# Performance work log

Measured on AMD Instinct MI355X. Metric: run time of the kernel, lower is better.

## Reference

```python
import jax, jax.numpy as jnp
import numpy as np

B, IN_F, OUT_F, H = 2048, 512, 512, 8
D = OUT_F // H  # head_dim = 64


def setup_inputs() -> dict:
    key = jax.random.key(0)
    ks = jax.random.split(key, 4)
    x = jax.random.normal(ks[0], (B, IN_F), dtype=jnp.float32)
    # learned params (per init_kwargs): nn.Linear(IN_F, OUT_F) and attention vector a
    W_w = jax.random.normal(ks[1], (OUT_F, IN_F), dtype=jnp.float32) * (1.0 / np.sqrt(IN_F))
    W_b = jnp.zeros((OUT_F,), dtype=jnp.float32)
    a = jax.random.normal(ks[2], (2 * D, 1), dtype=jnp.float32) * 0.1
    adj = jax.random.randint(ks[3], (B, B), 0, 2, dtype=jnp.int32)
    return {"x": x, "adj": adj, "W_w": W_w, "W_b": W_b, "a": a}


def reference(x, adj, W_w, W_b, a):
    Bn = x.shape[0]
    # h: [B, H, D]
    h = (x @ W_w.T + W_b).reshape(Bn, H, D)
    # decompose shared attention vector into src/dst halves (same for every head,
    # since torch code tiles a across heads via a.repeat(1, num_heads))
    a_src, a_dst = a[:D, 0], a[D:, 0]
    s_src = jnp.einsum('bhd,d->bh', h, a_src)  # [B, H] contribution of node i
    s_dst = jnp.einsum('bhd,d->bh', h, a_dst)  # [B, H] contribution of node j
    # e[i, j, h] = leakyrelu(h_i . a_src + h_j . a_dst)  -> [B, B, H]
    e = jax.nn.leaky_relu(s_src[:, None, :] + s_dst[None, :, :], negative_slope=0.2)
    e = jnp.where(adj[:, :, None] == 0, jnp.float32(-1e9), e)
    attn = jax.nn.softmax(e, axis=1)  # softmax over neighbors j (torch dim=1)
    # h_prime[i, h, :] = sum_j attn[i, j, h] * h[j, h, :]
    h_prime = jnp.einsum('ijh,jhd->ihd', attn, h).reshape(Bn, H * D)
    return jax.nn.elu(h_prime)
```

## Files before the change

### kernel.cpp

```cpp
#include <hip/hip_runtime.h>
#include <hip/hip_bf16.h>
#include <math.h>
#include <stdint.h>

#define BN 2048
#define KF 512
#define OF 512
#define NH 8
#define DD 64

typedef __attribute__((ext_vector_type(8))) short short8;
typedef __attribute__((ext_vector_type(4))) float f32x4;
typedef unsigned short ushortT;

static __device__ __forceinline__ ushortT bfcvt(float f) {
  __hip_bfloat16 h = __float2bfloat16(f);
  return *reinterpret_cast<ushortT*>(&h);
}
static __device__ __forceinline__ float bf2f(ushortT b) {
  return __uint_as_float(((unsigned)b) << 16);
}

#define SPLIT8(vsrc, dhi, dlo)                                        \
  {                                                                   \
    ushortT hi8[8], lo8[8];                                           \
    _Pragma("unroll") for (int i = 0; i < 8; ++i) {                   \
      hi8[i] = bfcvt((vsrc)[i]);                                      \
      lo8[i] = bfcvt((vsrc)[i] - bf2f(hi8[i]));                       \
    }                                                                 \
    (dhi) = *(const int4*)hi8;                                        \
    (dlo) = *(const int4*)lo8;                                        \
  }

__global__ __launch_bounds__(256, 2) void k_main(
    const float* __restrict__ x, const int* __restrict__ adj,
    const float* __restrict__ W, const float* __restrict__ Wb,
    const float* __restrict__ av,
    ushortT* __restrict__ hF, float* __restrict__ E12s, float* __restrict__ E12d,
    uint8_t* __restrict__ adjB) {
  __shared__ __align__(16) uint8_t smem[24576];
  __shared__ float sredS[2][32], sredD[2][32];

  const int t    = threadIdx.x;
  const int hh   = blockIdx.x;
  const int i0   = blockIdx.y * 32;
  const int b    = hh * 64 + blockIdx.y;
  const int lane = t & 63;
  const int wv   = t >> 6;
  const int mt   = wv & 1;
  const int nt   = wv >> 1;
  const int l15  = lane & 15;
  const int lq   = lane >> 4;

  {
    const int gtid = b * 256 + t;
#pragma unroll
    for (int it = 0; it < 4; ++it) {
      const int bidx = gtid + it * (512 * 256);
      const int4 v0 = *(const int4*)(adj + (size_t)bidx * 8);
      const int4 v1 = *(const int4*)(adj + (size_t)bidx * 8 + 4);
      unsigned m = (v0.x ? 1u : 0u) | (v0.y ? 2u : 0u) | (v0.z ? 4u : 0u) | (v0.w ? 8u : 0u)
                 | (v1.x ? 16u : 0u) | (v1.y ? 32u : 0u) | (v1.z ? 64u : 0u) | (v1.w ? 128u : 0u);
      adjB[bidx] = (uint8_t)m;
    }
  }

  ushortT* sAh = (ushortT*)smem;
  ushortT* sAl = sAh + 32 * 64;
  ushortT* sBh = sAl + 32 * 64;
  ushortT* sBl = sBh + 64 * 64;

  f32x4 acc[2] = {};
  const int srow = t >> 3, ss = t & 7;
  int4 aHi, aLo, bHi[2], bLo[2];

  {
    const float* xs = x + (size_t)(i0 + srow) * KF + ss * 8;
    float v[8];
    *(float4*)&v[0] = *(const float4*)xs;
    *(float4*)&v[4] = *(const float4*)(xs + 4);
    SPLIT8(v, aHi, aLo)
#pragma unroll
    for (int rp = 0; rp < 2; ++rp) {
      const int S = t + rp * 256, rw = S >> 3, s2 = S & 7;
      const float* wsrc = W + (size_t)(hh * 64 + rw) * KF + s2 * 8;
      float wv8[8];
      *(float4*)&wv8[0] = *(const float4*)wsrc;
      *(float4*)&wv8[4] = *(const float4*)(wsrc + 4);
      SPLIT8(wv8, bHi[rp], bLo[rp])
    }
  }

  for (int k0 = 0; k0 < 8; ++k0) {
    __syncthreads();
    {
      const int offA = srow * 64 + ((ss ^ (srow & 7)) * 8);
      *(int4*)&sAh[offA] = aHi;
      *(int4*)&sAl[offA] = aLo;
#pragma unroll
      for (int rp = 0; rp < 2; ++rp) {
        const int S = t + rp * 256, rw = S >> 3, s2 = S & 7;
        const int offB = rw * 64 + ((s2 ^ (rw & 7)) * 8);
        *(int4*)&sBh[offB] = bHi[rp];
        *(int4*)&sBl[offB] = bLo[rp];
      }
    }
    __syncthreads();
    if (k0 < 7) {
      const int kc = (k0 + 1) * 64;
      const float* xs = x + (size_t)(i0 + srow) * KF + kc + ss * 8;
      float v[8];
      *(float4*)&v[0] = *(const float4*)xs;
      *(float4*)&v[4] = *(const float4*)(xs + 4);
      SPLIT8(v, aHi, aLo)
#pragma unroll
      for (int rp = 0; rp < 2; ++rp) {
        const int S = t + rp * 256, rw = S >> 3, s2 = S & 7;
        const float* wsrc = W + (size_t)(hh * 64 + rw) * KF + kc + s2 * 8;
        float wv8[8];
        *(float4*)&wv8[0] = *(const float4*)wsrc;
        *(float4*)&wv8[4] = *(const float4*)(wsrc + 4);
        SPLIT8(wv8, bHi[rp], bLo[rp])
      }
    }
#pragma unroll
    for (int kb = 0; kb < 2; ++kb) {
      const int sc = kb * 4 + lq;
      const int arow = mt * 16 + l15;
      const int offA = arow * 64 + ((sc ^ (arow & 7)) * 8);
      const short8 afh = *(const short8*)&sAh[offA];
      const short8 afl = *(const short8*)&sAl[offA];
      const int br0 = nt * 32 + l15;
      const int br1 = br0 + 16;
      const int offB0 = br0 * 64 + ((sc ^ (br0 & 7)) * 8);
      const int offB1 = br1 * 64 + ((sc ^ (br1 & 7)) * 8);
      const short8 bh0 = *(const short8*)&sBh[offB0];
      const short8 bl0 = *(const short8*)&sBl[offB0];
      const short8 bh1 = *(const short8*)&sBh[offB1];
      const short8 bl1 = *(const short8*)&sBl[offB1];
      acc[0] = __builtin_amdgcn_mfma_f32_16x16x32_bf16(afh, bh0, acc[0], 0, 0, 0);
      acc[1] = __builtin_amdgcn_mfma_f32_16x16x32_bf16(afh, bh1, acc[1], 0, 0, 0);
      acc[0] = __builtin_amdgcn_mfma_f32_16x16x32_bf16(afh, bl0, acc[0], 0, 0, 0);
      acc[1] = __builtin_amdgcn_mfma_f32_16x16x32_bf16(afh, bl1, acc[1], 0, 0, 0);
      acc[0] = __builtin_amdgcn_mfma_f32_16x16x32_bf16(afl, bh0, acc[0], 0, 0, 0);
      acc[1] = __builtin_amdgcn_mfma_f32_16x16x32_bf16(afl, bh1, acc[1], 0, 0, 0);
    }
  }

  __syncthreads();
  ushortT* ldsT = (ushortT*)smem;
  float bias2[2], asv[2], adv[2];
#pragma unroll
  for (int bb = 0; bb < 2; ++bb) {
    const int fl = nt * 32 + bb * 16 + l15;
    bias2[bb] = Wb[hh * 64 + fl];
    asv[bb] = av[fl];
    adv[bb] = av[DD + fl];
  }
#pragma unroll
  for (int p = 0; p < 4; ++p) {
    float vs = 0.f, vd = 0.f;
#pragma unroll
    for (int bb = 0; bb < 2; ++bb) {
      const float hv = acc[bb][p] + bias2[bb];
      const ushortT hu = bfcvt(hv);
      vs = fmaf(hv, asv[bb], vs);
      vd = fmaf(hv, adv[bb], vd);
      ldsT[(nt * 32 + bb * 16 + l15) * 40 + mt * 16 + lq * 4 + p] = hu;
    }
    vs += __shfl_xor(vs, 1); vs += __shfl_xor(vs, 2);
    vs += __shfl_xor(vs, 4); vs += __shfl_xor(vs, 8);
    vd += __shfl_xor(vd, 1); vd += __shfl_xor(vd, 2);
    vd += __shfl_xor(vd, 4); vd += __shfl_xor(vd, 8);
    if (l15 == 0) {
      sredS[nt][mt * 16 + lq * 4 + p] = vs;
      sredD[nt][mt * 16 + lq * 4 + p] = vd;
    }
  }
  __syncthreads();
  if (t < 32) {
    const float s1 = sredS[0][t] + sredS[1][t];
    const float s2 = sredD[0][t] + sredD[1][t];
    const size_t gi = (size_t)hh * BN + i0 + t;
    float2 sv; sv.x = __expf(s1); sv.y = __expf(0.2f * s1);
    float2 dv; dv.x = __expf(s2); dv.y = __expf(0.2f * s2);
    *(float2*)&E12s[gi * 2] = sv;
    *(float2*)&E12d[gi * 2] = dv;
  }
  {
    const int n = t >> 6, ln = t & 63;
    const int4 v = *(const int4*)&ldsT[(n * 16 + (ln & 15)) * 40 + ((ln >> 4) * 8)];
    const size_t chunk = (((size_t)hh * 64 + blockIdx.y) * 4 + n) * 64 + ln;
    *(int4*)&hF[chunk * 8] = v;
  }
}

__global__ __launch_bounds__(512, 4) void k_attn(
    const ushortT* __restrict__ hF, const uint8_t* __restrict__ adjB,
    const float* __restrict__ E12s, const float* __restrict__ E12d,
    float* __restrict__ out) {
  __shared__ __align__(16) float e12[BN * 2];
  __shared__ __align__(16) float cbuf[4][2 * 16 * 68];
  __shared__ uint8_t abits[32 * 272];
  __shared__ float denP[8][2][16];

  const int t    = threadIdx.x;
  const int hh   = blockIdx.x;
  const int i0   = blockIdx.y * 32;
  const int lane = t & 63;
  const int wv   = t >> 6;
  const int l15  = lane & 15;
  const int lq   = lane >> 4;

  {
    const float4* g = (const float4*)(E12d + (size_t)hh * BN * 2);
    ((float4*)e12)[t]       = g[t];
    ((float4*)e12)[t + 512] = g[t + 512];
    const int r = t >> 4, pp = t & 15;
    *(int4*)(abits + r * 272 + pp * 16) =
        *(const int4*)(adjB + (size_t)(i0 + r) * 256 + pp * 16);
  }

  const float2 eiA = *(const float2*)&E12s[2 * ((size_t)hh * BN + i0 + l15)];
  const float2 eiB = *(const float2*)&E12s[2 * ((size_t)hh * BN + i0 + 16 + l15)];

  const short8 ones8 = {(short)0x3F80, (short)0x3F80, (short)0x3F80, (short)0x3F80,
                        (short)0x3F80, (short)0x3F80, (short)0x3F80, (short)0x3F80};

  const ushortT* hfb = hF + (size_t)hh * 131072 + (size_t)lane * 8;

  __syncthreads();

  const uint4 wA0 = *(const uint4*)(abits + l15 * 272 + wv * 32);
  const uint4 wA1 = *(const uint4*)(abits + l15 * 272 + wv * 32 + 16);
  const uint4 wB0 = *(const uint4*)(abits + (16 + l15) * 272 + wv * 32);
  const uint4 wB1 = *(const uint4*)(abits + (16 + l15) * 272 + wv * 32 + 16);
  const int lqs = lq * 8;

  f32x4 acc0[4] = {}, acc1[4] = {};
  f32x4 accd0 = {0.f, 0.f, 0.f, 0.f}, accd1 = {0.f, 0.f, 0.f, 0.f};

  const int jb0 = wv * 8;
  short8 bfA[4], bfB[4];
  {
    const ushortT* b0 = hfb + (size_t)(jb0 * 4) * 512;
#pragma unroll
    for (int n = 0; n < 4; ++n) bfA[n] = *(const short8*)(b0 + (size_t)n * 512);
  }

#define WSEL0(s) ((s)==0?wA0.x:(s)==1?wA0.y:(s)==2?wA0.z:(s)==3?wA0.w: \
                  (s)==4?wA1.x:(s)==5?wA1.y:(s)==6?wA1.z:wA1.w)
#define WSEL1(s) ((s)==0?wB0.x:(s)==1?wB0.y:(s)==2?wB0.z:(s)==3?wB0.w: \
                  (s)==4?wB1.x:(s)==5?wB1.y:(s)==6?wB1.z:wB1.w)

#define STEP(s, BCUR, BNXT)                                                        \
  {                                                                                \
    if ((s) < 7) {                                                                 \
      const ushortT* bn = hfb + (size_t)((jb0 + (s) + 1) * 4) * 512;               \
      _Pragma("unroll") for (int n = 0; n < 4; ++n)                                \
        BNXT[n] = *(const short8*)(bn + (size_t)n * 512);                          \
    }                                                                              \
    const int j0 = (jb0 + (s)) * 32 + lq * 8;                                      \
    const float* ep = &e12[j0 * 2];                                                \
    const float4 r0 = *(const float4*)(ep);                                        \
    const float4 r1 = *(const float4*)(ep + 4);                                    \
    const float4 r2 = *(const float4*)(ep + 8);                                    \
    const float4 r3 = *(const float4*)(ep + 12);                                   \
    const unsigned bb0 = (WSEL0(s) >> lqs) & 0xffu;                                \
    const unsigned bb1 = (WSEL1(s) >> lqs) & 0xffu;                                \
    unsigned pk0[4], pk1[4];                                                       \
    _Pragma("unroll") for (int q = 0; q < 4; ++q) {                                \
      const float4 rq = (q == 0) ? r0 : (q == 1) ? r1 : (q == 2) ? r2 : r3;        \
      float wa0 = fmaxf(eiA.x * rq.x, eiA.y * rq.y);                               \
      float wb0 = fmaxf(eiA.x * rq.z, eiA.y * rq.w);                               \
      float wa1 = fmaxf(eiB.x * rq.x, eiB.y * rq.y);                               \
      float wb1 = fmaxf(eiB.x * rq.z, eiB.y * rq.w);                               \
      wa0 = ((bb0 >> (2 * q)) & 1u) ? wa0 : 0.f;                                   \
      wb0 = ((bb0 >> (2 * q + 1)) & 1u) ? wb0 : 0.f;                               \
      wa1 = ((bb1 >> (2 * q)) & 1u) ? wa1 : 0.f;                                   \
      wb1 = ((bb1 >> (2 * q + 1)) & 1u) ? wb1 : 0.f;                               \
      asm("v_cvt_pk_bf16_f32 %0, %1, %2" : "=v"(pk0[q]) : "v"(wa0), "v"(wb0));     \
      asm("v_cvt_pk_bf16_f32 %0, %1, %2" : "=v"(pk1[q]) : "v"(wa1), "v"(wb1));     \
    }                                                                              \
    const short8 af0 = *(const short8*)pk0;                                        \
    const short8 af1 = *(const short8*)pk1;                                        \
    _Pragma("unroll") for (int n = 0; n < 4; ++n) {                                \
      acc0[n] = __builtin_amdgcn_mfma_f32_16x16x32_bf16(af0, BCUR[n], acc0[n], 0, 0, 0); \
      acc1[n] = __builtin_amdgcn_mfma_f32_16x16x32_bf16(af1, BCUR[n], acc1[n], 0, 0, 0); \
    }                                                                              \
    accd0 = __builtin_amdgcn_mfma_f32_16x16x32_bf16(af0, ones8, accd0, 0, 0, 0);   \
    accd1 = __builtin_amdgcn_mfma_f32_16x16x32_bf16(af1, ones8, accd1, 0, 0, 0);   \
  }

  STEP(0, bfA, bfB) STEP(1, bfB, bfA) STEP(2, bfA, bfB) STEP(3, bfB, bfA)
  STEP(4, bfA, bfB) STEP(5, bfB, bfA) STEP(6, bfA, bfB) STEP(7, bfB, bfA)
#undef STEP
#undef WSEL0
#undef WSEL1

  if (l15 == 0) {
#pragma unroll
    for (int p = 0; p < 4; ++p) {
      denP[wv][0][lq * 4 + p] = accd0[p];
      denP[wv][1][lq * 4 + p] = accd1[p];
    }
  }

#define CWRITE(buf)                                                     \
  _Pragma("unroll") for (int n = 0; n < 4; ++n)                         \
  _Pragma("unroll") for (int p = 0; p < 4; ++p) {                       \
    (buf)[(lq * 4 + p) * 68 + n * 16 + l15]      = acc0[n][p];          \
    (buf)[(16 + lq * 4 + p) * 68 + n * 16 + l15] = acc1[n][p];          \
  }
#define CADD(buf)                                                       \
  _Pragma("unroll") for (int n = 0; n < 4; ++n)                         \
  _Pragma("unroll") for (int p = 0; p < 4; ++p) {                       \
    acc0[n][p] += (buf)[(lq * 4 + p) * 68 + n * 16 + l15];              \
    acc1[n][p] += (buf)[(16 + lq * 4 + p) * 68 + n * 16 + l15];         \
  }

  if (wv >= 4) { CWRITE(cbuf[wv - 4]) }
  __syncthreads();
  if (wv < 4) {
    CADD(cbuf[wv])
    if (wv >= 2) { CWRITE(cbuf[wv]) }
  }
  __syncthreads();
  if (wv < 2) {
    CADD(cbuf[wv + 2])
    if (wv == 1) { CWRITE(cbuf[1]) }
  }
  __syncthreads();
  if (wv == 0) {
    CADD(cbuf[1])
    float dfin0[4], dfin1[4];
#pragma unroll
    for (int p = 0; p < 4; ++p) {
      const int row = lq * 4 + p;
      float d0 = 0.f, d1s = 0.f;
#pragma unroll
      for (int w = 0; w < 8; ++w) { d0 += denP[w][0][row]; d1s += denP[w][1][row]; }
      dfin0[p] = 1.f / d0;
      dfin1[p] = 1.f / d1s;
    }
#pragma unroll
    for (int n = 0; n < 4; ++n)
#pragma unroll
      for (int p = 0; p < 4; ++p) {
        float v0 = acc0[n][p] * dfin0[p];
        float v1 = acc1[n][p] * dfin1[p];
        v0 = v0 > 0.f ? v0 : expm1f(v0);
        v1 = v1 > 0.f ? v1 : expm1f(v1);
        out[(size_t)(i0 + lq * 4 + p) * OF + hh * 64 + n * 16 + l15] = v0;
        out[(size_t)(i0 + 16 + lq * 4 + p) * OF + hh * 64 + n * 16 + l15] = v1;
      }
  }
#undef CWRITE
#undef CADD
}

extern "C" void kernel_launch(void* const* d_in, const int* in_sizes, int n_in,
                              void* d_out, int out_size, void* d_ws, size_t ws_size,
                              hipStream_t stream) {
  const float* x  = (const float*)d_in[0];
  const int* adj  = (const int*)d_in[1];
  const float* Ww = (const float*)d_in[2];
  const float* Wb = (const float*)d_in[3];
  const float* a  = (const float*)d_in[4];
  float* outp = (float*)d_out;

  uint8_t* p = (uint8_t*)d_ws;
  ushortT* hF   = (ushortT*)(p + 0x000000);
  float*   E12d = (float*)  (p + 0x200000);
  float*   E12s = (float*)  (p + 0x220000);
  uint8_t* adjB =            p + 0x240000;

  k_main<<<dim3(NH, BN / 32), 256, 0, stream>>>(x, adj, Ww, Wb, a, hF, E12s, E12d, adjB);
  k_attn<<<dim3(NH, BN / 32), 512, 0, stream>>>(hF, adjB, E12s, E12d, outp);
}
```

Measured before the change: 33.06 us.

## Process 64 query rows per attention block to reuse each loaded h tile

Each k_attn block now covers 64 rows of i in four 16-row sub-tiles instead of 32, so every B fragment loaded from hF feeds four MFMA row tiles rather than two. The grid is halved, and the e12 staging load is amortized over twice as many rows. In exchange each thread holds twice the accumulators and adjacency words, the LDS reduction buffers double, and launch bounds drop to 2 blocks per CU, which lowers occupancy and the number of blocks available to fill the GPU.

```diff
diff --git a/kernel.cpp b/kernel.cpp
--- a/kernel.cpp
+++ b/kernel.cpp
@@ -195,18 +195,18 @@
   }
 }
 
-__global__ __launch_bounds__(512, 4) void k_attn(
+__global__ __launch_bounds__(512, 2) void k_attn(
     const ushortT* __restrict__ hF, const uint8_t* __restrict__ adjB,
     const float* __restrict__ E12s, const float* __restrict__ E12d,
     float* __restrict__ out) {
   __shared__ __align__(16) float e12[BN * 2];
-  __shared__ __align__(16) float cbuf[4][2 * 16 * 68];
-  __shared__ uint8_t abits[32 * 272];
-  __shared__ float denP[8][2][16];
+  __shared__ __align__(16) float cbuf[4][4 * 16 * 68];
+  __shared__ __align__(16) uint8_t abits[64 * 272];
+  __shared__ float denP[8][4][16];
 
   const int t    = threadIdx.x;
   const int hh   = blockIdx.x;
-  const int i0   = blockIdx.y * 32;
+  const int i0   = blockIdx.y * 64;
   const int lane = t & 63;
   const int wv   = t >> 6;
   const int l15  = lane & 15;
@@ -216,29 +216,36 @@
     const float4* g = (const float4*)(E12d + (size_t)hh * BN * 2);
     ((float4*)e12)[t]       = g[t];
     ((float4*)e12)[t + 512] = g[t + 512];
-    const int r = t >> 4, pp = t & 15;
-    *(int4*)(abits + r * 272 + pp * 16) =
-        *(const int4*)(adjB + (size_t)(i0 + r) * 256 + pp * 16);
-  }
-
-  const float2 eiA = *(const float2*)&E12s[2 * ((size_t)hh * BN + i0 + l15)];
-  const float2 eiB = *(const float2*)&E12s[2 * ((size_t)hh * BN + i0 + 16 + l15)];
+    const int r = t >> 3, pp = t & 7;
+    const int4* ga = (const int4*)(adjB + (size_t)(i0 + r) * 256 + pp * 32);
+    *(int4*)(abits + r * 272 + pp * 32)      = ga[0];
+    *(int4*)(abits + r * 272 + pp * 32 + 16) = ga[1];
+  }
+
+  float2 ei[4];
+#pragma unroll
+  for (int tl = 0; tl < 4; ++tl)
+    ei[tl] = *(const float2*)&E12s[2 * ((size_t)hh * BN + i0 + tl * 16 + l15)];
 
   const short8 ones8 = {(short)0x3F80, (short)0x3F80, (short)0x3F80, (short)0x3F80,
                         (short)0x3F80, (short)0x3F80, (short)0x3F80, (short)0x3F80};
 
   const ushortT* hfb = hF + (size_t)hh * 131072 + (size_t)lane * 8;
-
-  __syncthreads();
-
-  const uint4 wA0 = *(const uint4*)(abits + l15 * 272 + wv * 32);
-  const uint4 wA1 = *(const uint4*)(abits + l15 * 272 + wv * 32 + 16);
-  const uint4 wB0 = *(const uint4*)(abits + (16 + l15) * 272 + wv * 32);
-  const uint4 wB1 = *(const uint4*)(abits + (16 + l15) * 272 + wv * 32 + 16);
   const int lqs = lq * 8;
 
-  f32x4 acc0[4] = {}, acc1[4] = {};
-  f32x4 accd0 = {0.f, 0.f, 0.f, 0.f}, accd1 = {0.f, 0.f, 0.f, 0.f};
+  __syncthreads();
+
+  unsigned aw[4][8];
+#pragma unroll
+  for (int tl = 0; tl < 4; ++tl) {
+    const uint4 w0 = *(const uint4*)(abits + (tl * 16 + l15) * 272 + wv * 32);
+    const uint4 w1 = *(const uint4*)(abits + (tl * 16 + l15) * 272 + wv * 32 + 16);
+    aw[tl][0] = w0.x; aw[tl][1] = w0.y; aw[tl][2] = w0.z; aw[tl][3] = w0.w;
+    aw[tl][4] = w1.x; aw[tl][5] = w1.y; aw[tl][6] = w1.z; aw[tl][7] = w1.w;
+  }
+
+  f32x4 acc[4][4] = {};
+  f32x4 accd[4] = {};
 
   const int jb0 = wv * 8;
   short8 bfA[4], bfB[4];
@@ -247,11 +254,6 @@
 #pragma unroll
     for (int n = 0; n < 4; ++n) bfA[n] = *(const short8*)(b0 + (size_t)n * 512);
   }
-
-#define WSEL0(s) ((s)==0?wA0.x:(s)==1?wA0.y:(s)==2?wA0.z:(s)==3?wA0.w: \
-                  (s)==4?wA1.x:(s)==5?wA1.y:(s)==6?wA1.z:wA1.w)
-#define WSEL1(s) ((s)==0?wB0.x:(s)==1?wB0.y:(s)==2?wB0.z:(s)==3?wB0.w: \
-                  (s)==4?wB1.x:(s)==5?wB1.y:(s)==6?wB1.z:wB1.w)
 
 #define STEP(s, BCUR, BNXT)                                                        \
   {                                                                                \
@@ -260,64 +262,54 @@
       _Pragma("unroll") for (int n = 0; n < 4; ++n)                                \
         BNXT[n] = *(const short8*)(bn + (size_t)n * 512);                          \
     }                                                                              \
-    const int j0 = (jb0 + (s)) * 32 + lq * 8;                                      \
-    const float* ep = &e12[j0 * 2];                                                \
+    const float* ep = &e12[(((jb0 + (s)) * 32) + lq * 8) * 2];                     \
     const float4 r0 = *(const float4*)(ep);                                        \
     const float4 r1 = *(const float4*)(ep + 4);                                    \
     const float4 r2 = *(const float4*)(ep + 8);                                    \
     const float4 r3 = *(const float4*)(ep + 12);                                   \
-    const unsigned bb0 = (WSEL0(s) >> lqs) & 0xffu;                                \
-    const unsigned bb1 = (WSEL1(s) >> lqs) & 0xffu;                                \
-    unsigned pk0[4], pk1[4];                                                       \
-    _Pragma("unroll") for (int q = 0; q < 4; ++q) {                                \
-      const float4 rq = (q == 0) ? r0 : (q == 1) ? r1 : (q == 2) ? r2 : r3;        \
-      float wa0 = fmaxf(eiA.x * rq.x, eiA.y * rq.y);                               \
-      float wb0 = fmaxf(eiA.x * rq.z, eiA.y * rq.w);                               \
-      float wa1 = fmaxf(eiB.x * rq.x, eiB.y * rq.y);                               \
-      float wb1 = fmaxf(eiB.x * rq.z, eiB.y * rq.w);                               \
-      wa0 = ((bb0 >> (2 * q)) & 1u) ? wa0 : 0.f;                                   \
-      wb0 = ((bb0 >> (2 * q + 1)) & 1u) ? wb0 : 0.f;                               \
-      wa1 = ((bb1 >> (2 * q)) & 1u) ? wa1 : 0.f;                                   \
-      wb1 = ((bb1 >> (2 * q + 1)) & 1u) ? wb1 : 0.f;                               \
-      asm("v_cvt_pk_bf16_f32 %0, %1, %2" : "=v"(pk0[q]) : "v"(wa0), "v"(wb0));     \
-      asm("v_cvt_pk_bf16_f32 %0, %1, %2" : "=v"(pk1[q]) : "v"(wa1), "v"(wb1));     \
+    short8 af[4];                                                                  \
+    _Pragma("unroll") for (int tl = 0; tl < 4; ++tl) {                             \
+      const unsigned bb = (aw[tl][(s)] >> lqs) & 0xffu;                            \
+      unsigned pk[4];                                                              \
+      _Pragma("unroll") for (int q = 0; q < 4; ++q) {                              \
+        const float4 rq = (q == 0) ? r0 : (q == 1) ? r1 : (q == 2) ? r2 : r3;      \
+        float wa = fmaxf(ei[tl].x * rq.x, ei[tl].y * rq.y);                        \
+        float wb = fmaxf(ei[tl].x * rq.z, ei[tl].y * rq.w);                        \
+        wa = ((bb >> (2 * q)) & 1u) ? wa : 0.f;                                    \
+        wb = ((bb >> (2 * q + 1)) & 1u) ? wb : 0.f;                                \
+        asm("v_cvt_pk_bf16_f32 %0, %1, %2" : "=v"(pk[q]) : "v"(wa), "v"(wb));      \
+      }                                                                            \
+      af[tl] = *(const short8*)pk;                                                 \
     }                                                                              \
-    const short8 af0 = *(const short8*)pk0;                                        \
-    const short8 af1 = *(const short8*)pk1;                                        \
-    _Pragma("unroll") for (int n = 0; n < 4; ++n) {                                \
-      acc0[n] = __builtin_amdgcn_mfma_f32_16x16x32_bf16(af0, BCUR[n], acc0[n], 0, 0, 0); \
-      acc1[n] = __builtin_amdgcn_mfma_f32_16x16x32_bf16(af1, BCUR[n], acc1[n], 0, 0, 0); \
-    }                                                                              \
-    accd0 = __builtin_amdgcn_mfma_f32_16x16x32_bf16(af0, ones8, accd0, 0, 0, 0);   \
-    accd1 = __builtin_amdgcn_mfma_f32_16x16x32_bf16(af1, ones8, accd1, 0, 0, 0);   \
+    _Pragma("unroll") for (int n = 0; n < 4; ++n)                                  \
+      _Pragma("unroll") for (int tl = 0; tl < 4; ++tl)                             \
+        acc[tl][n] = __builtin_amdgcn_mfma_f32_16x16x32_bf16(af[tl], BCUR[n], acc[tl][n], 0, 0, 0); \
+    _Pragma("unroll") for (int tl = 0; tl < 4; ++tl)                               \
+      accd[tl] = __builtin_amdgcn_mfma_f32_16x16x32_bf16(af[tl], ones8, accd[tl], 0, 0, 0); \
   }
 
   STEP(0, bfA, bfB) STEP(1, bfB, bfA) STEP(2, bfA, bfB) STEP(3, bfB, bfA)
   STEP(4, bfA, bfB) STEP(5, bfB, bfA) STEP(6, bfA, bfB) STEP(7, bfB, bfA)
 #undef STEP
-#undef WSEL0
-#undef WSEL1
 
   if (l15 == 0) {
 #pragma unroll
-    for (int p = 0; p < 4; ++p) {
-      denP[wv][0][lq * 4 + p] = accd0[p];
-      denP[wv][1][lq * 4 + p] = accd1[p];
-    }
-  }
-
-#define CWRITE(buf)                                                     \
-  _Pragma("unroll") for (int n = 0; n < 4; ++n)                         \
-  _Pragma("unroll") for (int p = 0; p < 4; ++p) {                       \
-    (buf)[(lq * 4 + p) * 68 + n * 16 + l15]      = acc0[n][p];          \
-    (buf)[(16 + lq * 4 + p) * 68 + n * 16 + l15] = acc1[n][p];          \
-  }
-#define CADD(buf)                                                       \
-  _Pragma("unroll") for (int n = 0; n < 4; ++n)                         \
-  _Pragma("unroll") for (int p = 0; p < 4; ++p) {                       \
-    acc0[n][p] += (buf)[(lq * 4 + p) * 68 + n * 16 + l15];              \
-    acc1[n][p] += (buf)[(16 + lq * 4 + p) * 68 + n * 16 + l15];         \
-  }
+    for (int tl = 0; tl < 4; ++tl)
+#pragma unroll
+      for (int p = 0; p < 4; ++p)
+        denP[wv][tl][lq * 4 + p] = accd[tl][p];
+  }
+
+#define CWRITE(buf)                                                        \
+  _Pragma("unroll") for (int tl = 0; tl < 4; ++tl)                         \
+  _Pragma("unroll") for (int n = 0; n < 4; ++n)                            \
+  _Pragma("unroll") for (int p = 0; p < 4; ++p)                            \
+    (buf)[(tl * 16 + lq * 4 + p) * 68 + n * 16 + l15] = acc[tl][n][p];
+#define CADD(buf)                                                          \
+  _Pragma("unroll") for (int tl = 0; tl < 4; ++tl)                         \
+  _Pragma("unroll") for (int n = 0; n < 4; ++n)                            \
+  _Pragma("unroll") for (int p = 0; p < 4; ++p)                            \
+    acc[tl][n][p] += (buf)[(tl * 16 + lq * 4 + p) * 68 + n * 16 + l15];
 
   if (wv >= 4) { CWRITE(cbuf[wv - 4]) }
   __syncthreads();
@@ -333,27 +325,27 @@
   __syncthreads();
   if (wv == 0) {
     CADD(cbuf[1])
-    float dfin0[4], dfin1[4];
-#pragma unroll
-    for (int p = 0; p < 4; ++p) {
-      const int row = lq * 4 + p;
-      float d0 = 0.f, d1s = 0.f;
-#pragma unroll
-      for (int w = 0; w < 8; ++w) { d0 += denP[w][0][row]; d1s += denP[w][1][row]; }
-      dfin0[p] = 1.f / d0;
-      dfin1[p] = 1.f / d1s;
-    }
-#pragma unroll
-    for (int n = 0; n < 4; ++n)
+    float dfin[4][4];
+#pragma unroll
+    for (int tl = 0; tl < 4; ++tl)
 #pragma unroll
       for (int p = 0; p < 4; ++p) {
-        float v0 = acc0[n][p] * dfin0[p];
-        float v1 = acc1[n][p] * dfin1[p];
-        v0 = v0 > 0.f ? v0 : expm1f(v0);
-        v1 = v1 > 0.f ? v1 : expm1f(v1);
-        out[(size_t)(i0 + lq * 4 + p) * OF + hh * 64 + n * 16 + l15] = v0;
-        out[(size_t)(i0 + 16 + lq * 4 + p) * OF + hh * 64 + n * 16 + l15] = v1;
+        const int row = lq * 4 + p;
+        float d = 0.f;
+#pragma unroll
+        for (int w = 0; w < 8; ++w) d += denP[w][tl][row];
+        dfin[tl][p] = 1.f / d;
       }
+#pragma unroll
+    for (int tl = 0; tl < 4; ++tl)
+#pragma unroll
+      for (int n = 0; n < 4; ++n)
+#pragma unroll
+        for (int p = 0; p < 4; ++p) {
+          float v = acc[tl][n][p] * dfin[tl][p];
+          v = v > 0.f ? v : expm1f(v);
+          out[(size_t)(i0 + tl * 16 + lq * 4 + p) * OF + hh * 64 + n * 16 + l15] = v;
+        }
   }
 #undef CWRITE
 #undef CADD
@@ -376,5 +368,5 @@
   uint8_t* adjB =            p + 0x240000;
 
   k_main<<<dim3(NH, BN / 32), 256, 0, stream>>>(x, adj, Ww, Wb, a, hF, E12s, E12d, adjB);
-  k_attn<<<dim3(NH, BN / 32), 512, 0, stream>>>(hF, adjB, E12s, E12d, outp);
-}
+  k_attn<<<dim3(NH, BN / 64), 512, 0, stream>>>(hF, adjB, E12s, E12d, outp);
+}
```

New measurement: 37.37 us. 1.13x slower.
